# Performance work log

Measured on AMD Instinct MI355X. Metric: run time of the kernel, lower is better.

The kernel has to match this reference:

```python
import jax, jax.numpy as jnp
import numpy as np

WINDOW_SHAPE = (11, 11, 11)
CHANNELS = 1


def gaussian_nd(shape, sigma=1.0, mu=0.0):
    # n-dimensional gaussian kernel, identical to the torch source
    m = np.meshgrid(*[np.linspace(-1, 1, s) for s in shape])
    d = np.sqrt(np.sum([x * x for x in m], axis=0))
    g = np.exp(-((d - mu) ** 2 / (2.0 * sigma ** 2)))
    return g / np.sum(g)


def setup_inputs() -> dict:
    key = jax.random.key(0)
    k1, k2 = jax.random.split(key)
    shape = (2, 1, 96, 256, 256)  # N, C, D, H, W
    img1 = jax.random.uniform(k1, shape, dtype=jnp.float32)
    img2 = jax.random.uniform(k2, shape, dtype=jnp.float32)
    # depthwise window, shape (C, 1, 11, 11, 11) == (O, I/groups, D, H, W)
    w = jnp.asarray(gaussian_nd(WINDOW_SHAPE), dtype=jnp.float32)
    window = jnp.broadcast_to(w[None, None], (CHANNELS, 1) + WINDOW_SHAPE)
    return {"img1": img1, "img2": img2, "window": window}


def _blur(x, window):
    # depthwise 3D conv, padding=0 (VALID), groups=CHANNELS
    return jax.lax.conv_general_dilated(
        x, window, window_strides=(1, 1, 1), padding="VALID",
        dimension_numbers=("NCDHW", "OIDHW", "NCDHW"),
        feature_group_count=CHANNELS)


def reference(img1, img2, window):
    mu1 = _blur(img1, window)
    mu2 = _blur(img2, window)
    mu1_sq = mu1 * mu1
    mu2_sq = mu2 * mu2
    mu1_mu2 = mu1 * mu2
    sigma1_sq = _blur(img1 * img1, window) - mu1_sq
    sigma2_sq = _blur(img2 * img2, window) - mu2_sq
    sigma12 = _blur(img1 * img2, window) - mu1_mu2
    C1 = 0.01 ** 2
    C2 = 0.03 ** 2
    ssim_map = ((2 * mu1_mu2 + C1) * (2 * sigma12 + C2)
                / ((mu1_sq + mu2_sq + C1) * (sigma1_sq + sigma2_sq + C2)))
    # size_average=True -> scalar mean
    return jnp.mean(ssim_map)
```

## Files before the change

kernel.cpp:

```cpp
#include <hip/hip_runtime.h>
#include <hip/hip_fp16.h>

#define KW 11
#define NB 2
#define DI 96
#define HI 256
#define WI 256
#define DOUT 86
#define HOUT 246
#define WOUT 246
#define HT 16
#define WT 16
#define DCH 3
#define RR 26
#define HSZ (HI * WI)
#define SSIM_C1 1e-4f
#define SSIM_C2 9e-4f
#define NBLK (16 * 16 * NB * DCH)
#define ROW_SLOT 15
#define SLICE_SLOT (RR * ROW_SLOT)
#define PAIR_SLOT (2 * SLICE_SLOT)
#define SLICE_F (SLICE_SLOT * 4)
#define NSTG 4

typedef const unsigned int __attribute__((address_space(1)))* gp1_t;
typedef unsigned int __attribute__((address_space(3)))* lp3_t;
using f32x2 = __attribute__((ext_vector_type(2))) float;
using f32x4 = __attribute__((ext_vector_type(4))) float;

__device__ __forceinline__ void gl_lds16(const float* g, float* l) {
    __builtin_amdgcn_global_load_lds((gp1_t)(const void*)g, (lp3_t)(void*)l, 16, 0, 0);
}

__device__ __forceinline__ f32x2 pk_fma_s(f32x2 w, f32x2 x, f32x2 acc) {
    f32x2 d;
    asm("v_pk_fma_f32 %0, %1, %2, %3" : "=v"(d) : "s"(w), "v"(x), "v"(acc));
    return d;
}

__device__ __forceinline__ unsigned pk_fma_h(unsigned w, unsigned x, unsigned acc) {
    unsigned d;
    asm("v_pk_fma_f16 %0, %1, %2, %3" : "=v"(d) : "s"(w), "v"(x), "v"(acc));
    return d;
}

__device__ __forceinline__ unsigned pkrtz(float a, float b) {
    auto h = __builtin_amdgcn_cvt_pkrtz(a, b);
    return __builtin_bit_cast(unsigned, h);
}

__device__ __forceinline__ f32x2 h2f(unsigned u) {
    f32x2 r;
    r.x = __half2float(__ushort_as_half((unsigned short)(u & 0xffffu)));
    r.y = __half2float(__ushort_as_half((unsigned short)(u >> 16)));
    return r;
}

__device__ __forceinline__ float rfl(float x) {
    return __int_as_float(__builtin_amdgcn_readfirstlane(__float_as_int(x)));
}

template<int J>
__device__ __forceinline__ void acc_step(
    f32x2 (&AB)[KW], f32x2 (&PQ)[KW], const f32x2 (&w2)[KW],
    f32x2 f12, f32x2 f34, bool emit, f32x2& o12, f32x2& o34)
{
    #pragma unroll
    for (int p = 0; p < KW; ++p) {
        const int s = (J - p + KW) % KW;
        AB[s] = pk_fma_s(w2[p], f12, AB[s]);
        PQ[s] = pk_fma_s(w2[p], f34, PQ[s]);
    }
    const int C = (J + 1) % KW;
    if (emit) { o12 = AB[C]; o34 = PQ[C]; }
    AB[C] = (f32x2){0.f, 0.f};
    PQ[C] = (f32x2){0.f, 0.f};
}

static __global__ __launch_bounds__(256, 2) void ssim_main(
    const float* __restrict__ img1, const float* __restrict__ img2,
    const float* __restrict__ win, float* __restrict__ bsum)
{
    __shared__ __align__(16) float rawf[PAIR_SLOT * 4];
    __shared__ __align__(16) uint2 a4h[RR][17][2];
    float* const tmpw = (float*)a4h;
    float* const w1s  = (float*)a4h + 128;
    float* const red  = (float*)a4h + 140;

    const int t = threadIdx.x;
    const int bz = blockIdx.z;
    const int n = (bz >= DCH) ? 1 : 0;
    const int chunk = bz - n * DCH;
    const int d0 = (chunk == 0) ? 0 : (chunk == 1 ? 30 : 58);
    const int dpc = (chunk == 0) ? 30 : 28;
    const int NIT = (dpc + KW - 1) >> 1;
    const int h0 = blockIdx.y * HT, w0 = blockIdx.x * WT;

    if (t < 121) {
        const int i = t / KW, j = t - i * KW;
        const float* wp = win + i * (KW * KW) + j * KW;
        float s = 0.f;
        #pragma unroll
        for (int m = 0; m < KW; ++m) s += wp[m];
        tmpw[t] = s;
    }
    __syncthreads();
    if (t < KW) {
        float s = 0.f;
        #pragma unroll
        for (int j = 0; j < KW; ++j) s += tmpw[t * KW + j];
        w1s[t] = s;
    }
    __syncthreads();
    f32x2 w2[KW];
    unsigned whq[KW];
    #pragma unroll
    for (int k = 0; k < KW; ++k) {
        const float ws = rfl(w1s[k]);
        w2[k] = (f32x2){ws, ws};
        const unsigned hb = (unsigned)__half_as_ushort(__float2half(ws));
        whq[k] = __builtin_amdgcn_readfirstlane(hb | (hb << 16));
    }
    __syncthreads();

    const float* tp[NSTG];
    int tstr[NSTG];
    #pragma unroll
    for (int q = 0; q < NSTG; ++q) {
        const int u = t + 256 * q;
        const int sl = (u >= SLICE_SLOT) ? 1 : 0;
        const int v = u - sl * SLICE_SLOT;
        const int r = v / ROW_SLOT;
        const int rem = v - r * ROW_SLOT;
        const int half = (rem >= 7) ? 1 : 0;
        const int c = rem - 7 * half;
        const int gh = h0 + r, gw0 = w0 + 4 * c;
        const bool oob = (u >= PAIR_SLOT) || (c >= 7) || (gh >= HI) || (gw0 >= WI);
        const float* base = half ? img2 : img1;
        tp[q] = oob ? img1
                    : base + ((long)(n * DI + d0 + sl) * HSZ + (long)gh * WI + gw0);
        tstr[q] = oob ? 0 : 2 * HSZ;
    }
    #define STAGE() do { \
        float* db_ = &rawf[4 * t]; \
        gl_lds16(tp[0], db_);          tp[0] += tstr[0]; \
        gl_lds16(tp[1], db_ + 1024);   tp[1] += tstr[1]; \
        gl_lds16(tp[2], db_ + 2048);   tp[2] += tstr[2]; \
        if (t < PAIR_SLOT - 768) { gl_lds16(tp[3], db_ + 3072); tp[3] += tstr[3]; } \
    } while (0)

    f32x2 rAB[KW], rPQ[KW];
    #pragma unroll
    for (int p = 0; p < KW; ++p) { rAB[p] = (f32x2){0.f,0.f}; rPQ[p] = (f32x2){0.f,0.f}; }

    const int ty = t >> 4, tx = t & 15;
    const bool valid = (h0 + ty < HOUT) && (w0 + tx < WOUT);
    float partial = 0.f;

    const int paSl = (t >= 104) ? 1 : 0;
    const int paV  = (t < 208 ? t : 0) - paSl * 104;
    const int paCg = paV / 26;
    const int paR  = paV - paCg * 26;
    const float* const paRb = &rawf[paSl * SLICE_F + paR * 60];
    uint2* const paW = &a4h[paR][4 * paCg][paSl];

    auto phaseA = [&]() {
        f32x2 s12[4] = {{0.f,0.f},{0.f,0.f},{0.f,0.f},{0.f,0.f}};
        f32x2 s34[4] = {{0.f,0.f},{0.f,0.f},{0.f,0.f},{0.f,0.f}};
        #pragma unroll
        for (int q = 0; q < 4; ++q) {
            const f32x4 aq = *(const f32x4*)(paRb + 4 * (paCg + q));
            const f32x4 bq = *(const f32x4*)(paRb + 28 + 4 * (paCg + q));
            #pragma unroll
            for (int j = 0; j < 4; ++j) {
                const int m = 4 * q + j;
                if (m < 14) {
                    f32x2 pxy = (f32x2){aq[j], bq[j]};
                    pxy += (f32x2){-0.5f, -0.5f};
                    const float x = pxy.x, y = pxy.y;
                    const f32x2 pts = (f32x2){x * y, fmaf(x, x, y * y)};
                    #pragma unroll
                    for (int o = 0; o < 4; ++o) {
                        const int k = m - o;
                        if (k >= 0 && k <= 10) {
                            s12[o] = pk_fma_s(w2[k], pxy, s12[o]);
                            s34[o] = pk_fma_s(w2[k], pts, s34[o]);
                        }
                    }
                }
            }
        }
        #pragma unroll
        for (int o = 0; o < 4; ++o)
            paW[2 * o] = make_uint2(pkrtz(s12[o].x, s12[o].y),
                                    pkrtz(s34[o].x, s34[o].y));
    };

    STAGE();
    __syncthreads();

    int jj = 0;
    for (int i = 0; i < NIT; ++i) {
        if (t < 208) phaseA();
        __syncthreads();

        if (i + 1 < NIT) STAGE();

        unsigned ha12 = 0u, ha34 = 0u, hb12 = 0u, hb34 = 0u;
        #pragma unroll
        for (int kh = 0; kh < KW; ++kh) {
            const uint4 v = *(const uint4*)&a4h[ty + kh][tx][0];
            ha12 = pk_fma_h(whq[kh], v.x, ha12);
            ha34 = pk_fma_h(whq[kh], v.y, ha34);
            hb12 = pk_fma_h(whq[kh], v.z, hb12);
            hb34 = pk_fma_h(whq[kh], v.w, hb34);
        }
        const f32x2 fa12 = h2f(ha12), fa34 = h2f(ha34);
        const f32x2 fb12 = h2f(hb12), fb34 = h2f(hb34);

        const bool emit = (i >= 5);
        f32x2 oa12={0.f,0.f}, oa34={0.f,0.f}, ob12={0.f,0.f}, ob34={0.f,0.f};
        switch (jj) {
            #define CASE2(J) case J: \
                acc_step<J>(rAB, rPQ, w2, fa12, fa34, emit, oa12, oa34); \
                acc_step<(J+1)%KW>(rAB, rPQ, w2, fb12, fb34, emit, ob12, ob34); \
                break;
            CASE2(0) CASE2(1) CASE2(2) CASE2(3) CASE2(4) CASE2(5)
            CASE2(6) CASE2(7) CASE2(8) CASE2(9) CASE2(10)
            #undef CASE2
        }
        jj += 2; if (jj >= KW) jj -= KW;

        if (emit && valid) {
            {
                const float a = oa12.x, b = oa12.y;
                const float mu1 = a + 0.5f, mu2 = b + 0.5f;
                const float m11 = mu1 * mu1, m22 = mu2 * mu2, m12 = mu1 * mu2;
                const float s12c = oa34.x - a * b;
                const float ssum = oa34.y - a * a - b * b;
                const float num = (2.f * m12 + SSIM_C1) * (2.f * s12c + SSIM_C2);
                const float den = (m11 + m22 + SSIM_C1) * (ssum + SSIM_C2);
                partial += num * __builtin_amdgcn_rcpf(den);
            }
            {
                const float a = ob12.x, b = ob12.y;
                const float mu1 = a + 0.5f, mu2 = b + 0.5f;
                const float m11 = mu1 * mu1, m22 = mu2 * mu2, m12 = mu1 * mu2;
                const float s12c = ob34.x - a * b;
                const float ssum = ob34.y - a * a - b * b;
                const float num = (2.f * m12 + SSIM_C1) * (2.f * s12c + SSIM_C2);
                const float den = (m11 + m22 + SSIM_C1) * (ssum + SSIM_C2);
                partial += num * __builtin_amdgcn_rcpf(den);
            }
        }
        __syncthreads();
    }

    #pragma unroll
    for (int off = 32; off >= 1; off >>= 1)
        partial += __shfl_down(partial, off, 64);
    if ((t & 63) == 0) red[t >> 6] = partial;
    __syncthreads();
    if (t == 0) {
        bsum[(blockIdx.z * gridDim.y + blockIdx.y) * gridDim.x + blockIdx.x]
            = red[0] + red[1] + red[2] + red[3];
    }
}

static __global__ __launch_bounds__(256) void ssim_reduce(
    const float* __restrict__ bsum, float* __restrict__ out)
{
    __shared__ double red[4];
    const int t = threadIdx.x;
    double s = 0.0;
    for (int i = t; i < NBLK; i += 256) s += (double)bsum[i];
    #pragma unroll
    for (int off = 32; off >= 1; off >>= 1)
        s += __shfl_down(s, off, 64);
    if ((t & 63) == 0) red[t >> 6] = s;
    __syncthreads();
    if (t == 0) {
        const double tot = red[0] + red[1] + red[2] + red[3];
        out[0] = (float)(tot / (double)((long)NB * DOUT * HOUT * WOUT));
    }
}

extern "C" void kernel_launch(void* const* d_in, const int* in_sizes, int n_in,
                              void* d_out, int out_size, void* d_ws, size_t ws_size,
                              hipStream_t stream)
{
    const float* img1 = (const float*)d_in[0];
    const float* img2 = (const float*)d_in[1];
    const float* win  = (const float*)d_in[2];
    float* out  = (float*)d_out;
    float* bsum = (float*)d_ws;

    dim3 grid(16, 16, NB * DCH);
    ssim_main<<<grid, 256, 0, stream>>>(img1, img2, win, bsum);
    ssim_reduce<<<1, 256, 0, stream>>>(bsum, out);
}
```

Measured before the change: 101.0 us.

## Move depth-axis accumulation to packed fp16 and restructure LDS staging layout

```diff
diff --git a/kernel.cpp b/kernel.cpp
--- a/kernel.cpp
+++ b/kernel.cpp
@@ -17,11 +17,8 @@
 #define SSIM_C1 1e-4f
 #define SSIM_C2 9e-4f
 #define NBLK (16 * 16 * NB * DCH)
-#define ROW_SLOT 15
-#define SLICE_SLOT (RR * ROW_SLOT)
-#define PAIR_SLOT (2 * SLICE_SLOT)
-#define SLICE_F (SLICE_SLOT * 4)
-#define NSTG 4
+#define RAW1_SLOT 364
+#define RAW_SLOT 728
 
 typedef const unsigned int __attribute__((address_space(1)))* gp1_t;
 typedef unsigned int __attribute__((address_space(3)))* lp3_t;
@@ -61,27 +58,27 @@
 }
 
 template<int J>
-__device__ __forceinline__ void acc_step(
-    f32x2 (&AB)[KW], f32x2 (&PQ)[KW], const f32x2 (&w2)[KW],
-    f32x2 f12, f32x2 f34, bool emit, f32x2& o12, f32x2& o34)
+__device__ __forceinline__ void acc_step_h(
+    unsigned (&AB)[KW], unsigned (&PQ)[KW], const unsigned (&wh)[KW],
+    unsigned f12, unsigned f34, bool emit, unsigned& o12, unsigned& o34)
 {
     #pragma unroll
     for (int p = 0; p < KW; ++p) {
         const int s = (J - p + KW) % KW;
-        AB[s] = pk_fma_s(w2[p], f12, AB[s]);
-        PQ[s] = pk_fma_s(w2[p], f34, PQ[s]);
+        AB[s] = pk_fma_h(wh[p], f12, AB[s]);
+        PQ[s] = pk_fma_h(wh[p], f34, PQ[s]);
     }
     const int C = (J + 1) % KW;
     if (emit) { o12 = AB[C]; o34 = PQ[C]; }
-    AB[C] = (f32x2){0.f, 0.f};
-    PQ[C] = (f32x2){0.f, 0.f};
+    AB[C] = 0u;
+    PQ[C] = 0u;
 }
 
 static __global__ __launch_bounds__(256, 2) void ssim_main(
     const float* __restrict__ img1, const float* __restrict__ img2,
     const float* __restrict__ win, float* __restrict__ bsum)
 {
-    __shared__ __align__(16) float rawf[PAIR_SLOT * 4];
+    __shared__ __align__(16) float rawf[RAW_SLOT * 4];
     __shared__ __align__(16) uint2 a4h[RR][17][2];
     float* const tmpw = (float*)a4h;
     float* const w1s  = (float*)a4h + 128;
@@ -123,35 +120,32 @@
     }
     __syncthreads();
 
-    const float* tp[NSTG];
-    int tstr[NSTG];
-    #pragma unroll
-    for (int q = 0; q < NSTG; ++q) {
-        const int u = t + 256 * q;
-        const int sl = (u >= SLICE_SLOT) ? 1 : 0;
-        const int v = u - sl * SLICE_SLOT;
-        const int r = v / ROW_SLOT;
-        const int rem = v - r * ROW_SLOT;
-        const int half = (rem >= 7) ? 1 : 0;
-        const int c = rem - 7 * half;
+    unsigned soff[2];
+    #pragma unroll
+    for (int q = 0; q < 2; ++q) {
+        const int s = t + 256 * q;
+        const int sl = (s >= 182) ? 1 : 0;
+        const int v = (s < RAW1_SLOT ? s : 0) - sl * 182;
+        const int r = v / 7;
+        const int c = v - 7 * r;
         const int gh = h0 + r, gw0 = w0 + 4 * c;
-        const bool oob = (u >= PAIR_SLOT) || (c >= 7) || (gh >= HI) || (gw0 >= WI);
-        const float* base = half ? img2 : img1;
-        tp[q] = oob ? img1
-                    : base + ((long)(n * DI + d0 + sl) * HSZ + (long)gh * WI + gw0);
-        tstr[q] = oob ? 0 : 2 * HSZ;
+        const bool oob = (s >= RAW1_SLOT) || (gh >= HI) || (gw0 >= WI);
+        soff[q] = oob ? 0u
+                      : (unsigned)((((n * DI + d0 + sl) * HSZ) + gh * WI + gw0) * 4);
     }
     #define STAGE() do { \
-        float* db_ = &rawf[4 * t]; \
-        gl_lds16(tp[0], db_);          tp[0] += tstr[0]; \
-        gl_lds16(tp[1], db_ + 1024);   tp[1] += tstr[1]; \
-        gl_lds16(tp[2], db_ + 2048);   tp[2] += tstr[2]; \
-        if (t < PAIR_SLOT - 768) { gl_lds16(tp[3], db_ + 3072); tp[3] += tstr[3]; } \
+        gl_lds16((const float*)((const char*)img1 + soff[0]), &rawf[4 * t]); \
+        gl_lds16((const float*)((const char*)img2 + soff[0]), &rawf[RAW1_SLOT * 4 + 4 * t]); \
+        if (t < RAW1_SLOT - 256) { \
+            gl_lds16((const float*)((const char*)img1 + soff[1]), &rawf[1024 + 4 * t]); \
+            gl_lds16((const float*)((const char*)img2 + soff[1]), &rawf[RAW1_SLOT * 4 + 1024 + 4 * t]); \
+        } \
+        soff[0] += 8 * HSZ; soff[1] += 8 * HSZ; \
     } while (0)
 
-    f32x2 rAB[KW], rPQ[KW];
-    #pragma unroll
-    for (int p = 0; p < KW; ++p) { rAB[p] = (f32x2){0.f,0.f}; rPQ[p] = (f32x2){0.f,0.f}; }
+    unsigned rABh[KW], rPQh[KW];
+    #pragma unroll
+    for (int p = 0; p < KW; ++p) { rABh[p] = 0u; rPQh[p] = 0u; }
 
     const int ty = t >> 4, tx = t & 15;
     const bool valid = (h0 + ty < HOUT) && (w0 + tx < WOUT);
@@ -161,7 +155,8 @@
     const int paV  = (t < 208 ? t : 0) - paSl * 104;
     const int paCg = paV / 26;
     const int paR  = paV - paCg * 26;
-    const float* const paRb = &rawf[paSl * SLICE_F + paR * 60];
+    const float* const paA = &rawf[(paSl * 182 + paR * 7) * 4];
+    const float* const paB = paA + RAW1_SLOT * 4;
     uint2* const paW = &a4h[paR][4 * paCg][paSl];
 
     auto phaseA = [&]() {
@@ -169,8 +164,8 @@
         f32x2 s34[4] = {{0.f,0.f},{0.f,0.f},{0.f,0.f},{0.f,0.f}};
         #pragma unroll
         for (int q = 0; q < 4; ++q) {
-            const f32x4 aq = *(const f32x4*)(paRb + 4 * (paCg + q));
-            const f32x4 bq = *(const f32x4*)(paRb + 28 + 4 * (paCg + q));
+            const f32x4 aq = *(const f32x4*)(paA + 4 * (paCg + q));
+            const f32x4 bq = *(const f32x4*)(paB + 4 * (paCg + q));
             #pragma unroll
             for (int j = 0; j < 4; ++j) {
                 const int m = 4 * q + j;
@@ -215,15 +210,13 @@
             hb12 = pk_fma_h(whq[kh], v.z, hb12);
             hb34 = pk_fma_h(whq[kh], v.w, hb34);
         }
-        const f32x2 fa12 = h2f(ha12), fa34 = h2f(ha34);
-        const f32x2 fb12 = h2f(hb12), fb34 = h2f(hb34);
 
         const bool emit = (i >= 5);
-        f32x2 oa12={0.f,0.f}, oa34={0.f,0.f}, ob12={0.f,0.f}, ob34={0.f,0.f};
+        unsigned oa12u = 0u, oa34u = 0u, ob12u = 0u, ob34u = 0u;
         switch (jj) {
             #define CASE2(J) case J: \
-                acc_step<J>(rAB, rPQ, w2, fa12, fa34, emit, oa12, oa34); \
-                acc_step<(J+1)%KW>(rAB, rPQ, w2, fb12, fb34, emit, ob12, ob34); \
+                acc_step_h<J>(rABh, rPQh, whq, ha12, ha34, emit, oa12u, oa34u); \
+                acc_step_h<(J+1)%KW>(rABh, rPQh, whq, hb12, hb34, emit, ob12u, ob34u); \
                 break;
             CASE2(0) CASE2(1) CASE2(2) CASE2(3) CASE2(4) CASE2(5)
             CASE2(6) CASE2(7) CASE2(8) CASE2(9) CASE2(10)
@@ -233,21 +226,23 @@
 
         if (emit && valid) {
             {
-                const float a = oa12.x, b = oa12.y;
+                const f32x2 v12 = h2f(oa12u), v34 = h2f(oa34u);
+                const float a = v12.x, b = v12.y;
                 const float mu1 = a + 0.5f, mu2 = b + 0.5f;
                 const float m11 = mu1 * mu1, m22 = mu2 * mu2, m12 = mu1 * mu2;
-                const float s12c = oa34.x - a * b;
-                const float ssum = oa34.y - a * a - b * b;
+                const float s12c = v34.x - a * b;
+                const float ssum = v34.y - a * a - b * b;
                 const float num = (2.f * m12 + SSIM_C1) * (2.f * s12c + SSIM_C2);
                 const float den = (m11 + m22 + SSIM_C1) * (ssum + SSIM_C2);
                 partial += num * __builtin_amdgcn_rcpf(den);
             }
             {
-                const float a = ob12.x, b = ob12.y;
+                const f32x2 v12 = h2f(ob12u), v34 = h2f(ob34u);
+                const float a = v12.x, b = v12.y;
                 const float mu1 = a + 0.5f, mu2 = b + 0.5f;
                 const float m11 = mu1 * mu1, m22 = mu2 * mu2, m12 = mu1 * mu2;
-                const float s12c = ob34.x - a * b;
-                const float ssum = ob34.y - a * a - b * b;
+                const float s12c = v34.x - a * b;
+                const float ssum = v34.y - a * a - b * b;
                 const float num = (2.f * m12 + SSIM_C1) * (2.f * s12c + SSIM_C2);
                 const float den = (m11 + m22 + SSIM_C1) * (ssum + SSIM_C2);
                 partial += num * __builtin_amdgcn_rcpf(den);
```

Measured after the change: 90.28 us. -10.6%, faster.
